# Kernel optimization log

Measured on AMD Instinct MI355X. Metric: run time of the kernel, lower is better.

Reference implementation:

```python
import jax, jax.numpy as jnp
import numpy as np

NEG_SLOPE = 0.2

def setup_inputs() -> dict:
    key = jax.random.key(0)
    ks = jax.random.split(key, 10)
    N, E, F, H, C, NC, G = 50000, 800000, 256, 8, 32, 10, 128
    x = jax.random.normal(ks[0], (N, F), jnp.float32)
    W1 = jax.random.normal(ks[1], (F, H * C), jnp.float32) * (1.0 / np.sqrt(F))
    a_src1 = jax.random.normal(ks[2], (H, C), jnp.float32) * 0.1
    a_dst1 = jax.random.normal(ks[3], (H, C), jnp.float32) * 0.1
    b1 = jnp.zeros((H * C,), jnp.float32)
    W2 = jax.random.normal(ks[4], (H * C, NC), jnp.float32) * (1.0 / np.sqrt(H * C))
    a_src2 = jax.random.normal(ks[5], (1, NC), jnp.float32) * 0.1
    a_dst2 = jax.random.normal(ks[6], (1, NC), jnp.float32) * 0.1
    b2 = jnp.zeros((NC,), jnp.float32)
    edge_index = jax.random.randint(ks[7], (2, E), 0, N, jnp.int64)
    batch = jnp.sort(jax.random.randint(ks[8], (N,), 0, G, jnp.int64))
    return {"x": x, "W1": W1, "a_src1": a_src1, "a_dst1": a_dst1, "b1": b1,
            "W2": W2, "a_src2": a_src2, "a_dst2": a_dst2, "b2": b2,
            "edge_index": edge_index, "batch": batch}


def gat_conv(x, W, a_src, a_dst, b, src, dst, concat):
    # x: [N,F] -> h: [N,H,C]
    N = x.shape[0]
    H, C = a_src.shape
    h = (x @ W).reshape(N, H, C)
    alpha_s = jnp.einsum('nhc,hc->nh', h, a_src)  # [N,H]
    alpha_d = jnp.einsum('nhc,hc->nh', h, a_dst)  # [N,H]
    e = jax.nn.leaky_relu(alpha_s[src] + alpha_d[dst], NEG_SLOPE)  # [E,H]
    # segment softmax over edges sharing the same destination node
    m = jax.ops.segment_max(e, dst, num_segments=N)
    ex = jnp.exp(e - m[dst])
    s = jax.ops.segment_sum(ex, dst, num_segments=N)
    alpha = ex / s[dst]
    msg = h[src] * alpha[:, :, None]  # [E,H,C]
    out = jax.ops.segment_sum(msg, dst, num_segments=N)  # [N,H,C]
    out = out.reshape(N, H * C) if concat else out.mean(axis=1)
    return out + b


def reference(x, W1, a_src1, a_dst1, b1, W2, a_src2, a_dst2, b2, edge_index, batch):
    N = x.shape[0]
    G = 128
    loop = jnp.arange(N, dtype=edge_index.dtype)
    src = jnp.concatenate([edge_index[0], loop])  # add self loops (PyG default)
    dst = jnp.concatenate([edge_index[1], loop])
    # dropout layers are identity at inference (training=False)
    h = jax.nn.elu(gat_conv(x, W1, a_src1, a_dst1, b1, src, dst, concat=True))
    out = gat_conv(h, W2, a_src2, a_dst2, b2, src, dst, concat=False)  # [N,NC]
    # global mean pool over graphs
    sums = jax.ops.segment_sum(out, batch, num_segments=G)
    cnt = jax.ops.segment_sum(jnp.ones((N,), out.dtype), batch, num_segments=G)
    return sums / jnp.maximum(cnt, 1.0)[:, None]
```

## Files before the change

kernel.cpp:

```cpp
#include <hip/hip_runtime.h>
#include <hip/hip_bf16.h>
#include <math.h>

#define N_NODES 50000
#define N_EDGES 800000
#define E_TOT   (N_EDGES + N_NODES)
#define NCLS 10
#define NGRP 128

#define NBKT 196
#define EPB  1024
#define NB1  ((E_TOT + EPB - 1) / EPB)

typedef __attribute__((ext_vector_type(8))) short bf16x8;
typedef __attribute__((ext_vector_type(4))) float f32x4;
typedef __attribute__((ext_vector_type(2))) float f32x2;

static __device__ __forceinline__ ushort f2bf(float f) {
  union { float f; unsigned u; } v; v.f = f;
  unsigned r = v.u + 0x7fffu + ((v.u >> 16) & 1u);
  return (ushort)(r >> 16);
}
static __device__ __forceinline__ unsigned char enc8(float v) {
  int p = __builtin_amdgcn_cvt_pk_fp8_f32(v, v, 0, false);
  return (unsigned char)(p & 0xFF);
}
static __device__ __forceinline__ void fma4p(float w, unsigned u, f32x2* a) {
  f32x2 w2; w2[0] = w; w2[1] = w;
  a[0] += w2 * __builtin_amdgcn_cvt_pk_f32_fp8(u, false);
  a[1] += w2 * __builtin_amdgcn_cvt_pk_f32_fp8(u, true);
}

#define CAST_BLOCKS 2048
#define NX4 (N_NODES * 64)
#define W1T_BASE CAST_BLOCKS
#define W2T_BASE (W1T_BASE + 64)
#define WA_BASE  (W2T_BASE + 1)
#define HIST_BASE (WA_BASE + 1)
#define PREP_BLOCKS (HIST_BASE + NB1)

__global__ __launch_bounds__(256) void prep_kernel(const float4* __restrict__ X4,
                                                   ushort4* __restrict__ Xb,
                                                   const float* __restrict__ W1,
                                                   ushort* __restrict__ W1t,
                                                   const float* __restrict__ W2,
                                                   ushort* __restrict__ W2tp,
                                                   const float* __restrict__ asrc1,
                                                   const float* __restrict__ adst1,
                                                   const int* __restrict__ ei,
                                                   int* __restrict__ histg) {
  int b = blockIdx.x;
  int tid = threadIdx.x;
  if (b < CAST_BLOCKS) {
    for (int i = b * 256 + tid; i < NX4; i += CAST_BLOCKS * 256) {
      float4 v = X4[i];
      ushort4 o;
      o.x = f2bf(v.x); o.y = f2bf(v.y); o.z = f2bf(v.z); o.w = f2bf(v.w);
      Xb[i] = o;
    }
  } else if (b < W2T_BASE) {
    __shared__ float t[32][33];
    int bb = b - W1T_BASE;
    int k0 = (bb >> 3) * 32, n0 = (bb & 7) * 32;
    int tx = tid & 31, ty = tid >> 5;
    for (int r = 0; r < 32; r += 8)
      t[ty + r][tx] = W1[(k0 + ty + r) * 256 + n0 + tx];
    __syncthreads();
    for (int r = 0; r < 32; r += 8)
      W1t[(n0 + ty + r) * 256 + k0 + tx] = f2bf(t[tx][ty + r]);
  } else if (b == W2T_BASE) {
    int k = tid;
#pragma unroll
    for (int c = 0; c < 16; ++c)
      W2tp[c * 256 + k] = (c < NCLS) ? f2bf(W2[k * NCLS + c]) : (ushort)0;
  } else if (b == WA_BASE) {
    int k = tid;
    const float* wrow = W1 + k * 256;
#pragma unroll
    for (int h = 0; h < 8; ++h) {
      float s = 0.f, d = 0.f;
#pragma unroll
      for (int c = 0; c < 32; ++c) {
        float w = wrow[h * 32 + c];
        s += w * asrc1[h * 32 + c];
        d += w * adst1[h * 32 + c];
      }
      W1t[(256 + h) * 256 + k] = f2bf(s);
      W1t[(264 + h) * 256 + k] = f2bf(d);
    }
  } else {
    __shared__ int h[NBKT];
    int bb = b - HIST_BASE;
    for (int j = tid; j < NBKT; j += 256) h[j] = 0;
    __syncthreads();
    int base = bb * EPB;
#pragma unroll
    for (int t = 0; t < 4; ++t) {
      int i = base + t * 256 + tid;
      if (i < E_TOT) {
        int d = (i < N_EDGES) ? ei[N_EDGES + i] : (i - N_EDGES);
        atomicAdd(&h[d >> 8], 1);
      }
    }
    __syncthreads();
    for (int j = tid; j < NBKT; j += 256) histg[j * NB1 + bb] = h[j];
  }
}

#define GEMM_BLOCKS ((N_NODES + 63) / 64)

__global__ __launch_bounds__(256) void gemm1_mfma(const ushort* __restrict__ Xb,
                                                  const ushort* __restrict__ W1t,
                                                  unsigned char* __restrict__ h1f8,
                                                  float* __restrict__ as1,
                                                  float* __restrict__ ad1) {
  __shared__ ushort As[32][64][8];
  int wid = threadIdx.x >> 6, lane = threadIdx.x & 63;
  int r = lane & 15, kg = lane >> 4;
  int m0 = blockIdx.x * 64;
  int n0 = wid * 64;
  bool extra = (wid == 3);

  {
    int mi = wid;
    int row = m0 + mi * 16 + r;
    if (row >= N_NODES) row = 0;
    const ushort* src = Xb + (size_t)row * 256 + kg * 8;
    bf16x8 v0 = *reinterpret_cast<const bf16x8*>(src);
    bf16x8 v1 = *reinterpret_cast<const bf16x8*>(src + 32);
    bf16x8 v2 = *reinterpret_cast<const bf16x8*>(src + 64);
    bf16x8 v3 = *reinterpret_cast<const bf16x8*>(src + 96);
    bf16x8 v4 = *reinterpret_cast<const bf16x8*>(src + 128);
    bf16x8 v5 = *reinterpret_cast<const bf16x8*>(src + 160);
    bf16x8 v6 = *reinterpret_cast<const bf16x8*>(src + 192);
    bf16x8 v7 = *reinterpret_cast<const bf16x8*>(src + 224);
    *reinterpret_cast<bf16x8*>(&As[mi * 8 + 0][lane][0]) = v0;
    *reinterpret_cast<bf16x8*>(&As[mi * 8 + 1][lane][0]) = v1;
    *reinterpret_cast<bf16x8*>(&As[mi * 8 + 2][lane][0]) = v2;
    *reinterpret_cast<bf16x8*>(&As[mi * 8 + 3][lane][0]) = v3;
    *reinterpret_cast<bf16x8*>(&As[mi * 8 + 4][lane][0]) = v4;
    *reinterpret_cast<bf16x8*>(&As[mi * 8 + 5][lane][0]) = v5;
    *reinterpret_cast<bf16x8*>(&As[mi * 8 + 6][lane][0]) = v6;
    *reinterpret_cast<bf16x8*>(&As[mi * 8 + 7][lane][0]) = v7;
  }
  __syncthreads();

  f32x4 acc[4][4];
  f32x4 accE[4];
#pragma unroll
  for (int mi = 0; mi < 4; ++mi) {
#pragma unroll
    for (int ni = 0; ni < 4; ++ni) acc[mi][ni] = 0;
    accE[mi] = 0;
  }

  const ushort* bptr[4];
#pragma unroll
  for (int ni = 0; ni < 4; ++ni)
    bptr[ni] = W1t + (size_t)(n0 + ni * 16 + r) * 256 + kg * 8;
  const ushort* bptrE = W1t + (size_t)(256 + r) * 256 + kg * 8;

#pragma unroll 2
  for (int ks = 0; ks < 8; ++ks) {
    int k0 = ks * 32;
    bf16x8 a[4], b[4], bE;
#pragma unroll
    for (int ni = 0; ni < 4; ++ni)
      b[ni] = *reinterpret_cast<const bf16x8*>(bptr[ni] + k0);
    if (extra) bE = *reinterpret_cast<const bf16x8*>(bptrE + k0);
#pragma unroll
    for (int mi = 0; mi < 4; ++mi)
      a[mi] = *reinterpret_cast<const bf16x8*>(&As[mi * 8 + ks][lane][0]);
#pragma unroll
    for (int mi = 0; mi < 4; ++mi) {
#pragma unroll
      for (int ni = 0; ni < 4; ++ni)
        acc[mi][ni] = __builtin_amdgcn_mfma_f32_16x16x32_bf16(a[mi], b[ni], acc[mi][ni], 0, 0, 0);
      if (extra)
        accE[mi] = __builtin_amdgcn_mfma_f32_16x16x32_bf16(a[mi], bE, accE[mi], 0, 0, 0);
    }
  }

#pragma unroll
  for (int mi = 0; mi < 4; ++mi) {
#pragma unroll
    for (int q = 0; q < 4; ++q) {
      int row = m0 + mi * 16 + kg * 4 + q;
      if (row < N_NODES) {
#pragma unroll
        for (int ni = 0; ni < 4; ++ni)
          h1f8[(size_t)row * 256 + n0 + ni * 16 + r] = enc8(acc[mi][ni][q]);
        if (extra) {
          float* dst = (r < 8) ? (as1 + row * 8 + r) : (ad1 + row * 8 + (r & 7));
          *dst = accE[mi][q];
        }
      }
    }
  }
}

__global__ __launch_bounds__(256) void k_scan(int* __restrict__ histg,
                                              int* __restrict__ tot) {
  __shared__ int sh[256];
  int b = blockIdx.x, tid = threadIdx.x;
  int carry = 0;
  for (int c = 0; c < (NB1 + 255) / 256; ++c) {
    int j = c * 256 + tid;
    int v = (j < NB1) ? histg[b * NB1 + j] : 0;
    sh[tid] = v;
    __syncthreads();
    for (int d = 1; d < 256; d <<= 1) {
      int t = (tid >= d) ? sh[tid - d] : 0;
      __syncthreads();
      sh[tid] += t;
      __syncthreads();
    }
    if (j < NB1) histg[b * NB1 + j] = carry + sh[tid] - v;
    carry += sh[255];
    __syncthreads();
  }
  if (tid == 0) tot[b] = carry;
}

__global__ __launch_bounds__(256) void k_base(const int* __restrict__ tot,
                                              int* __restrict__ baseg) {
  __shared__ int sh[256];
  int tid = threadIdx.x;
  int v = (tid < NBKT) ? tot[tid] : 0;
  sh[tid] = v;
  __syncthreads();
  for (int d = 1; d < 256; d <<= 1) {
    int t = (tid >= d) ? sh[tid - d] : 0;
    __syncthreads();
    sh[tid] += t;
    __syncthreads();
  }
  if (tid < NBKT) baseg[tid] = sh[tid] - v;
  if (tid == 255) baseg[NBKT] = sh[255];
}

__global__ __launch_bounds__(256) void k_place(const int* __restrict__ ei,
                                               const int* __restrict__ histg,
                                               const int* __restrict__ baseg,
                                               unsigned int* __restrict__ cs) {
  __shared__ int h[NBKT];
  __shared__ int basec[NBKT];
  int tid = threadIdx.x;
  for (int j = tid; j < NBKT; j += 256) {
    h[j] = 0;
    basec[j] = baseg[j] + histg[j * NB1 + blockIdx.x];
  }
  __syncthreads();
  int base = blockIdx.x * EPB;
#pragma unroll
  for (int t = 0; t < 4; ++t) {
    int i = base + t * 256 + tid;
    if (i < E_TOT) {
      int s = (i < N_EDGES) ? ei[i] : (i - N_EDGES);
      int d = (i < N_EDGES) ? ei[N_EDGES + i] : (i - N_EDGES);
      int bk = d >> 8;
      int r = atomicAdd(&h[bk], 1);
      cs[basec[bk] + r] = ((unsigned)d << 16) | (unsigned)s;
    }
  }
}

__global__ __launch_bounds__(256) void k_fine(const unsigned int* __restrict__ cs,
                                              const int* __restrict__ baseg,
                                              int* __restrict__ csr,
                                              int* __restrict__ off) {
  __shared__ int cnt[256];
  __shared__ int sh[256];
  __shared__ int scn[256];
  __shared__ int cur[256];
  int b = blockIdx.x, tid = threadIdx.x;
  int lo = baseg[b], hi = baseg[b + 1];
  cnt[tid] = 0;
  cur[tid] = 0;
  __syncthreads();
  for (int i = lo + tid; i < hi; i += 256) atomicAdd(&cnt[(cs[i] >> 16) & 255], 1);
  __syncthreads();
  int v = cnt[tid];
  sh[tid] = v;
  __syncthreads();
  for (int d = 1; d < 256; d <<= 1) {
    int t = (tid >= d) ? sh[tid - d] : 0;
    __syncthreads();
    sh[tid] += t;
    __syncthreads();
  }
  scn[tid] = sh[tid] - v;
  int idx = b * 256 + tid;
  if (idx <= N_NODES) off[idx] = lo + scn[tid];
  __syncthreads();
  for (int i = lo + tid; i < hi; i += 256) {
    unsigned e = cs[i];
    int dl = (e >> 16) & 255;
    int r = atomicAdd(&cur[dl], 1);
    csr[lo + scn[dl] + r] = (int)((e & 0xFFFFu) << 8);
  }
}

__global__ __launch_bounds__(256) void agg1_kernel(const unsigned char* __restrict__ h1f8,
                                                   const float* __restrict__ as1,
                                                   const float* __restrict__ ad1,
                                                   const int* __restrict__ off,
                                                   const int* __restrict__ csr,
                                                   const float* __restrict__ b1,
                                                   ushort* __restrict__ h2b) {
  int n = (blockIdx.x * 256 + threadIdx.x) >> 6;
  int lane = threadIdx.x & 63;
  int p0 = off[n], p1 = off[n + 1];

  int sl = lane >> 4;
  int cl = lane & 15;
  int cb = cl * 16;
  int h = cl >> 1;
  float ad = ad1[n * 8 + h];

  float ssum = 0.f;
  f32x2 acc2[8];
#pragma unroll
  for (int j = 0; j < 8; ++j) { acc2[j][0] = 0.f; acc2[j][1] = 0.f; }

  int p = p0 + sl;
  for (; p + 4 < p1; p += 8) {
    int vA = csr[p], vB = csr[p + 4];
    float eA = as1[(vA >> 5) + h] + ad;
    float eB = as1[(vB >> 5) + h] + ad;
    uint4 rA = *reinterpret_cast<const uint4*>(h1f8 + vA + cb);
    uint4 rB = *reinterpret_cast<const uint4*>(h1f8 + vB + cb);
    eA = eA > 0.f ? eA : 0.2f * eA;
    eB = eB > 0.f ? eB : 0.2f * eB;
    float wA = __expf(eA), wB = __expf(eB);
    ssum += wA + wB;
    fma4p(wA, rA.x, acc2 + 0); fma4p(wB, rB.x, acc2 + 0);
    fma4p(wA, rA.y, acc2 + 2); fma4p(wB, rB.y, acc2 + 2);
    fma4p(wA, rA.z, acc2 + 4); fma4p(wB, rB.z, acc2 + 4);
    fma4p(wA, rA.w, acc2 + 6); fma4p(wB, rB.w, acc2 + 6);
  }
  for (; p < p1; p += 4) {
    int vA = csr[p];
    float eA = as1[(vA >> 5) + h] + ad;
    uint4 rA = *reinterpret_cast<const uint4*>(h1f8 + vA + cb);
    eA = eA > 0.f ? eA : 0.2f * eA;
    float wA = __expf(eA);
    ssum += wA;
    fma4p(wA, rA.x, acc2 + 0);
    fma4p(wA, rA.y, acc2 + 2);
    fma4p(wA, rA.z, acc2 + 4);
    fma4p(wA, rA.w, acc2 + 6);
  }

  ssum += __shfl_xor(ssum, 16); ssum += __shfl_xor(ssum, 32);
#pragma unroll
  for (int j = 0; j < 8; ++j) {
    acc2[j][0] += __shfl_xor(acc2[j][0], 16);
    acc2[j][0] += __shfl_xor(acc2[j][0], 32);
    acc2[j][1] += __shfl_xor(acc2[j][1], 16);
    acc2[j][1] += __shfl_xor(acc2[j][1], 32);
  }

  if (sl == 0) {
    float inv = 1.f / ssum;
    float o[16];
    float4 b0 = *reinterpret_cast<const float4*>(b1 + cb);
    float4 b1v = *reinterpret_cast<const float4*>(b1 + cb + 4);
    float4 b2v = *reinterpret_cast<const float4*>(b1 + cb + 8);
    float4 b3v = *reinterpret_cast<const float4*>(b1 + cb + 12);
    float bb[16] = {b0.x, b0.y, b0.z, b0.w, b1v.x, b1v.y, b1v.z, b1v.w,
                    b2v.x, b2v.y, b2v.z, b2v.w, b3v.x, b3v.y, b3v.z, b3v.w};
#pragma unroll
    for (int c = 0; c < 16; ++c) {
      float v = acc2[c >> 1][c & 1] * inv + bb[c];
      o[c] = v > 0.f ? v : __expf(v) - 1.f;
    }
    int4 o0, o1;
    o0.x = (int)(((unsigned)f2bf(o[1]) << 16) | f2bf(o[0]));
    o0.y = (int)(((unsigned)f2bf(o[3]) << 16) | f2bf(o[2]));
    o0.z = (int)(((unsigned)f2bf(o[5]) << 16) | f2bf(o[4]));
    o0.w = (int)(((unsigned)f2bf(o[7]) << 16) | f2bf(o[6]));
    o1.x = (int)(((unsigned)f2bf(o[9]) << 16) | f2bf(o[8]));
    o1.y = (int)(((unsigned)f2bf(o[11]) << 16) | f2bf(o[10]));
    o1.z = (int)(((unsigned)f2bf(o[13]) << 16) | f2bf(o[12]));
    o1.w = (int)(((unsigned)f2bf(o[15]) << 16) | f2bf(o[14]));
    *reinterpret_cast<int4*>(h2b + (size_t)n * 256 + cb) = o0;
    *reinterpret_cast<int4*>(h2b + (size_t)n * 256 + cb + 8) = o1;
  }
}

__global__ __launch_bounds__(256) void proj2_mfma(const ushort* __restrict__ h2b,
                                                  const ushort* __restrict__ W2tp,
                                                  const float* __restrict__ asrc2,
                                                  const float* __restrict__ adst2,
                                                  float* __restrict__ pj2p,
                                                  float* __restrict__ as2,
                                                  float* __restrict__ ad2) {
  int wid = threadIdx.x >> 6, lane = threadIdx.x & 63;
  int r = lane & 15, kg = lane >> 4;
  int rb = blockIdx.x * 64 + wid * 16;
  int row_a = rb + r;
  if (row_a >= N_NODES) row_a = 0;
  const ushort* ap = h2b + (size_t)row_a * 256 + kg * 8;
  const ushort* bp = W2tp + (size_t)r * 256 + kg * 8;
  f32x4 acc = 0;
#pragma unroll
  for (int k0 = 0; k0 < 256; k0 += 32)
    acc = __builtin_amdgcn_mfma_f32_16x16x32_bf16(
        *reinterpret_cast<const bf16x8*>(ap + k0),
        *reinterpret_cast<const bf16x8*>(bp + k0), acc, 0, 0, 0);

  float av = (r < NCLS) ? asrc2[r] : 0.f;
  float dv = (r < NCLS) ? adst2[r] : 0.f;
#pragma unroll
  for (int q = 0; q < 4; ++q) {
    int row = rb + kg * 4 + q;
    float v = acc[q];
    if (row < N_NODES) pj2p[row * 16 + r] = v;
    float s = v * av, d = v * dv;
    s += __shfl_xor(s, 1); s += __shfl_xor(s, 2); s += __shfl_xor(s, 4); s += __shfl_xor(s, 8);
    d += __shfl_xor(d, 1); d += __shfl_xor(d, 2); d += __shfl_xor(d, 4); d += __shfl_xor(d, 8);
    if (r == 0 && row < N_NODES) { as2[row] = s; ad2[row] = d; }
  }
}

__global__ __launch_bounds__(256) void agg2_kernel(const float* __restrict__ pj2p,
                                                   const float* __restrict__ as2,
                                                   const float* __restrict__ ad2,
                                                   const int* __restrict__ off,
                                                   const int* __restrict__ csr,
                                                   const float* __restrict__ b2,
                                                   float* __restrict__ out2p) {
  int n = (blockIdx.x * 256 + threadIdx.x) >> 6;
  int lane = threadIdx.x & 63;
  int p0 = off[n], p1 = off[n + 1];
  float ad = ad2[n];
  int es = lane >> 4, c = lane & 15;
  float ssum = 0.f, acc = 0.f;
  int p = p0 + es;
  for (; p + 12 < p1; p += 16) {
    int v0 = csr[p], v1 = csr[p + 4], v2 = csr[p + 8], v3 = csr[p + 12];
    float e0 = as2[v0 >> 8] + ad, e1 = as2[v1 >> 8] + ad;
    float e2 = as2[v2 >> 8] + ad, e3 = as2[v3 >> 8] + ad;
    float q0 = pj2p[(v0 >> 4) + c], q1 = pj2p[(v1 >> 4) + c];
    float q2 = pj2p[(v2 >> 4) + c], q3 = pj2p[(v3 >> 4) + c];
    e0 = e0 > 0.f ? e0 : 0.2f * e0;
    e1 = e1 > 0.f ? e1 : 0.2f * e1;
    e2 = e2 > 0.f ? e2 : 0.2f * e2;
    e3 = e3 > 0.f ? e3 : 0.2f * e3;
    float w0 = __expf(e0), w1 = __expf(e1), w2 = __expf(e2), w3 = __expf(e3);
    ssum += (w0 + w1) + (w2 + w3);
    acc += (w0 * q0 + w1 * q1) + (w2 * q2 + w3 * q3);
  }
  for (; p < p1; p += 4) {
    int vA = csr[p];
    float eA = as2[vA >> 8] + ad;
    float qA = pj2p[(vA >> 4) + c];
    eA = eA > 0.f ? eA : 0.2f * eA;
    float wA = __expf(eA);
    ssum += wA;
    acc += wA * qA;
  }
  acc += __shfl_xor(acc, 16); acc += __shfl_xor(acc, 32);
  ssum += __shfl_xor(ssum, 16); ssum += __shfl_xor(ssum, 32);
  if (lane < 16) {
    float bc = (lane < NCLS) ? b2[lane] : 0.f;
    out2p[n * 16 + lane] = acc / ssum + bc;
  }
}

__global__ __launch_bounds__(256) void pool_kernel(const float* __restrict__ out2p,
                                                   const int* __restrict__ batch,
                                                   float* __restrict__ outp) {
  __shared__ float red[256];
  int g = blockIdx.x;
  int lo = 0, hi = N_NODES;
  while (lo < hi) { int mid = (lo + hi) >> 1; if (batch[mid] < g) lo = mid + 1; else hi = mid; }
  int start = lo;
  hi = N_NODES;
  while (lo < hi) { int mid = (lo + hi) >> 1; if (batch[mid] < g + 1) lo = mid + 1; else hi = mid; }
  int end = lo;
  int t = threadIdx.x;
  int c = t & 15, nsl = t >> 4;
  float loc = 0.f;
  for (int nn = start + nsl; nn < end; nn += 16) loc += out2p[nn * 16 + c];
  red[t] = loc;
  __syncthreads();
  for (int s = 128; s >= 16; s >>= 1) {
    if (t < s) red[t] += red[t + s];
    __syncthreads();
  }
  if (t < NCLS) {
    float denom = fmaxf((float)(end - start), 1.f);
    outp[g * NCLS + t] = red[t] / denom;
  }
}

extern "C" void kernel_launch(void* const* d_in, const int* in_sizes, int n_in,
                              void* d_out, int out_size, void* d_ws, size_t ws_size,
                              hipStream_t stream) {
  const float* x      = (const float*)d_in[0];
  const float* W1     = (const float*)d_in[1];
  const float* a_src1 = (const float*)d_in[2];
  const float* a_dst1 = (const float*)d_in[3];
  const float* b1     = (const float*)d_in[4];
  const float* W2     = (const float*)d_in[5];
  const float* a_src2 = (const float*)d_in[6];
  const float* a_dst2 = (const float*)d_in[7];
  const float* b2     = (const float*)d_in[8];
  const int*   ei     = (const int*)d_in[9];
  const int*   batch  = (const int*)d_in[10];

  char* ws = (char*)d_ws;
  size_t o = 0;
  auto alloc = [&](size_t bytes) {
    char* p = ws + o;
    o = (o + bytes + 255) & ~(size_t)255;
    return p;
  };
  ushort* xb   = (ushort*)alloc((size_t)N_NODES * 256 * 2);
  ushort* w1t  = (ushort*)alloc((size_t)272 * 256 * 2);
  ushort* w2tp = (ushort*)alloc((size_t)16 * 256 * 2);
  unsigned char* h1f8 = (unsigned char*)alloc((size_t)N_NODES * 256);
  ushort* h2b  = (ushort*)alloc((size_t)N_NODES * 256 * 2);
  float* as1   = (float*)alloc((size_t)N_NODES * 8 * 4);
  float* ad1   = (float*)alloc((size_t)N_NODES * 8 * 4);
  float* pj2p  = (float*)alloc((size_t)N_NODES * 16 * 4);
  float* as2   = (float*)alloc((size_t)N_NODES * 4);
  float* ad2   = (float*)alloc((size_t)N_NODES * 4);
  float* out2p = (float*)alloc((size_t)N_NODES * 16 * 4);
  int*   histg = (int*)alloc((size_t)NBKT * NB1 * 4);
  int*   tot   = (int*)alloc((size_t)NBKT * 4);
  int*   baseg = (int*)alloc((size_t)(NBKT + 1) * 4);
  unsigned int* cs = (unsigned int*)alloc((size_t)E_TOT * 4);
  int*   csr   = (int*)alloc((size_t)E_TOT * 4);
  int*   off   = (int*)alloc((size_t)(N_NODES + 1) * 4);

  prep_kernel<<<PREP_BLOCKS, 256, 0, stream>>>((const float4*)x, (ushort4*)xb,
                                               W1, w1t, W2, w2tp, a_src1, a_dst1,
                                               ei, histg);
  gemm1_mfma<<<GEMM_BLOCKS, 256, 0, stream>>>(xb, w1t, h1f8, as1, ad1);

  k_scan<<<NBKT, 256, 0, stream>>>(histg, tot);
  k_base<<<1, 256, 0, stream>>>(tot, baseg);
  k_place<<<NB1, 256, 0, stream>>>(ei, histg, baseg, cs);
  k_fine<<<NBKT, 256, 0, stream>>>(cs, baseg, csr, off);

  agg1_kernel<<<N_NODES / 4, 256, 0, stream>>>(h1f8, as1, ad1, off, csr, b1, h2b);
  proj2_mfma<<<GEMM_BLOCKS, 256, 0, stream>>>(h2b, w2tp, a_src2, a_dst2,
                                              pj2p, as2, ad2);
  agg2_kernel<<<N_NODES / 4, 256, 0, stream>>>(pj2p, as2, ad2, off, csr, b2, out2p);
  pool_kernel<<<NGRP, 256, 0, stream>>>(out2p, batch, (float*)d_out);
}
```

Before: 264.9 us.

## Fuse edge placement into GEMM launch and fold bucket-base scan into consumers

Removes the separate k_base and k_place launches. Each placement block and each k_fine block now recomputes the small 196-entry prefix scan of bucket totals, and the placement blocks are appended to the GEMM1 grid so the sort scatter can overlap with the MFMA work. The agg1 accumulation also switches from packed f32x2 FMAs to scalar FMAs on a 16-float array. The cost is redundant scans per block and mixed block types in one grid, which may affect occupancy or register use of the GEMM path.

```diff
diff --git a/kernel.cpp b/kernel.cpp
--- a/kernel.cpp
+++ b/kernel.cpp
@@ -25,10 +25,10 @@
   int p = __builtin_amdgcn_cvt_pk_fp8_f32(v, v, 0, false);
   return (unsigned char)(p & 0xFF);
 }
-static __device__ __forceinline__ void fma4p(float w, unsigned u, f32x2* a) {
-  f32x2 w2; w2[0] = w; w2[1] = w;
-  a[0] += w2 * __builtin_amdgcn_cvt_pk_f32_fp8(u, false);
-  a[1] += w2 * __builtin_amdgcn_cvt_pk_f32_fp8(u, true);
+static __device__ __forceinline__ void fma4(float w, unsigned u, float* a) {
+  f32x2 lo = __builtin_amdgcn_cvt_pk_f32_fp8(u, false);
+  f32x2 hi = __builtin_amdgcn_cvt_pk_f32_fp8(u, true);
+  a[0] += w * lo[0]; a[1] += w * lo[1]; a[2] += w * hi[0]; a[3] += w * hi[1];
 }
 
 #define CAST_BLOCKS 2048
@@ -107,15 +107,80 @@
   }
 }
 
+__global__ __launch_bounds__(256) void k_scan(int* __restrict__ histg,
+                                              int* __restrict__ tot) {
+  __shared__ int sh[256];
+  int b = blockIdx.x, tid = threadIdx.x;
+  int carry = 0;
+  for (int c = 0; c < (NB1 + 255) / 256; ++c) {
+    int j = c * 256 + tid;
+    int v = (j < NB1) ? histg[b * NB1 + j] : 0;
+    sh[tid] = v;
+    __syncthreads();
+    for (int d = 1; d < 256; d <<= 1) {
+      int t = (tid >= d) ? sh[tid - d] : 0;
+      __syncthreads();
+      sh[tid] += t;
+      __syncthreads();
+    }
+    if (j < NB1) histg[b * NB1 + j] = carry + sh[tid] - v;
+    carry += sh[255];
+    __syncthreads();
+  }
+  if (tid == 0) tot[b] = carry;
+}
+
 #define GEMM_BLOCKS ((N_NODES + 63) / 64)
-
-__global__ __launch_bounds__(256) void gemm1_mfma(const ushort* __restrict__ Xb,
+#define GP_BLOCKS (GEMM_BLOCKS + NB1)
+
+__global__ __launch_bounds__(256) void gemm_place(const ushort* __restrict__ Xb,
                                                   const ushort* __restrict__ W1t,
                                                   unsigned char* __restrict__ h1f8,
                                                   float* __restrict__ as1,
-                                                  float* __restrict__ ad1) {
+                                                  float* __restrict__ ad1,
+                                                  const int* __restrict__ ei,
+                                                  const int* __restrict__ histg,
+                                                  const int* __restrict__ tot,
+                                                  unsigned int* __restrict__ cs) {
   __shared__ ushort As[32][64][8];
-  int wid = threadIdx.x >> 6, lane = threadIdx.x & 63;
+  int tid = threadIdx.x;
+
+  if (blockIdx.x >= GEMM_BLOCKS) {
+    int bb = blockIdx.x - GEMM_BLOCKS;
+    int* L = (int*)As;
+    int* h     = L;
+    int* basec = L + 256;
+    int* sh    = L + 512;
+    int tv = (tid < NBKT) ? tot[tid] : 0;
+    sh[tid] = tv;
+    __syncthreads();
+    for (int d = 1; d < 256; d <<= 1) {
+      int t = (tid >= d) ? sh[tid - d] : 0;
+      __syncthreads();
+      sh[tid] += t;
+      __syncthreads();
+    }
+    if (tid < NBKT) {
+      basec[tid] = (sh[tid] - tv) + histg[tid * NB1 + bb];
+      h[tid] = 0;
+    }
+    __syncthreads();
+    int base = bb * EPB;
+#pragma unroll
+    for (int t = 0; t < 4; ++t) {
+      int i = base + t * 256 + tid;
+      if (i < E_TOT) {
+        int s = (i < N_EDGES) ? ei[i] : (i - N_EDGES);
+        int d = (i < N_EDGES) ? ei[N_EDGES + i] : (i - N_EDGES);
+        int bk = d >> 8;
+        int r = atomicAdd(&h[bk], 1);
+        cs[basec[bk] + r] = ((unsigned)d << 16) | (unsigned)s;
+      }
+    }
+    return;
+  }
+
+  int wid = tid >> 6, lane = tid & 63;
   int r = lane & 15, kg = lane >> 4;
   int m0 = blockIdx.x * 64;
   int n0 = wid * 64;
@@ -199,74 +264,8 @@
   }
 }
 
-__global__ __launch_bounds__(256) void k_scan(int* __restrict__ histg,
-                                              int* __restrict__ tot) {
-  __shared__ int sh[256];
-  int b = blockIdx.x, tid = threadIdx.x;
-  int carry = 0;
-  for (int c = 0; c < (NB1 + 255) / 256; ++c) {
-    int j = c * 256 + tid;
-    int v = (j < NB1) ? histg[b * NB1 + j] : 0;
-    sh[tid] = v;
-    __syncthreads();
-    for (int d = 1; d < 256; d <<= 1) {
-      int t = (tid >= d) ? sh[tid - d] : 0;
-      __syncthreads();
-      sh[tid] += t;
-      __syncthreads();
-    }
-    if (j < NB1) histg[b * NB1 + j] = carry + sh[tid] - v;
-    carry += sh[255];
-    __syncthreads();
-  }
-  if (tid == 0) tot[b] = carry;
-}
-
-__global__ __launch_bounds__(256) void k_base(const int* __restrict__ tot,
-                                              int* __restrict__ baseg) {
-  __shared__ int sh[256];
-  int tid = threadIdx.x;
-  int v = (tid < NBKT) ? tot[tid] : 0;
-  sh[tid] = v;
-  __syncthreads();
-  for (int d = 1; d < 256; d <<= 1) {
-    int t = (tid >= d) ? sh[tid - d] : 0;
-    __syncthreads();
-    sh[tid] += t;
-    __syncthreads();
-  }
-  if (tid < NBKT) baseg[tid] = sh[tid] - v;
-  if (tid == 255) baseg[NBKT] = sh[255];
-}
-
-__global__ __launch_bounds__(256) void k_place(const int* __restrict__ ei,
-                                               const int* __restrict__ histg,
-                                               const int* __restrict__ baseg,
-                                               unsigned int* __restrict__ cs) {
-  __shared__ int h[NBKT];
-  __shared__ int basec[NBKT];
-  int tid = threadIdx.x;
-  for (int j = tid; j < NBKT; j += 256) {
-    h[j] = 0;
-    basec[j] = baseg[j] + histg[j * NB1 + blockIdx.x];
-  }
-  __syncthreads();
-  int base = blockIdx.x * EPB;
-#pragma unroll
-  for (int t = 0; t < 4; ++t) {
-    int i = base + t * 256 + tid;
-    if (i < E_TOT) {
-      int s = (i < N_EDGES) ? ei[i] : (i - N_EDGES);
-      int d = (i < N_EDGES) ? ei[N_EDGES + i] : (i - N_EDGES);
-      int bk = d >> 8;
-      int r = atomicAdd(&h[bk], 1);
-      cs[basec[bk] + r] = ((unsigned)d << 16) | (unsigned)s;
-    }
-  }
-}
-
 __global__ __launch_bounds__(256) void k_fine(const unsigned int* __restrict__ cs,
-                                              const int* __restrict__ baseg,
+                                              const int* __restrict__ tot,
                                               int* __restrict__ csr,
                                               int* __restrict__ off) {
   __shared__ int cnt[256];
@@ -274,7 +273,20 @@
   __shared__ int scn[256];
   __shared__ int cur[256];
   int b = blockIdx.x, tid = threadIdx.x;
-  int lo = baseg[b], hi = baseg[b + 1];
+
+  int tv = (tid < NBKT) ? tot[tid] : 0;
+  sh[tid] = tv;
+  __syncthreads();
+  for (int d = 1; d < 256; d <<= 1) {
+    int t = (tid >= d) ? sh[tid - d] : 0;
+    __syncthreads();
+    sh[tid] += t;
+    __syncthreads();
+  }
+  int hi = sh[b];
+  int lo = hi - tot[b];
+  __syncthreads();
+
   cnt[tid] = 0;
   cur[tid] = 0;
   __syncthreads();
@@ -319,9 +331,7 @@
   float ad = ad1[n * 8 + h];
 
   float ssum = 0.f;
-  f32x2 acc2[8];
-#pragma unroll
-  for (int j = 0; j < 8; ++j) { acc2[j][0] = 0.f; acc2[j][1] = 0.f; }
+  float acc[16] = {};
 
   int p = p0 + sl;
   for (; p + 4 < p1; p += 8) {
@@ -334,10 +344,10 @@
     eB = eB > 0.f ? eB : 0.2f * eB;
     float wA = __expf(eA), wB = __expf(eB);
     ssum += wA + wB;
-    fma4p(wA, rA.x, acc2 + 0); fma4p(wB, rB.x, acc2 + 0);
-    fma4p(wA, rA.y, acc2 + 2); fma4p(wB, rB.y, acc2 + 2);
-    fma4p(wA, rA.z, acc2 + 4); fma4p(wB, rB.z, acc2 + 4);
-    fma4p(wA, rA.w, acc2 + 6); fma4p(wB, rB.w, acc2 + 6);
+    fma4(wA, rA.x, acc);      fma4(wB, rB.x, acc);
+    fma4(wA, rA.y, acc + 4);  fma4(wB, rB.y, acc + 4);
+    fma4(wA, rA.z, acc + 8);  fma4(wB, rB.z, acc + 8);
+    fma4(wA, rA.w, acc + 12); fma4(wB, rB.w, acc + 12);
   }
   for (; p < p1; p += 4) {
     int vA = csr[p];
@@ -346,19 +356,17 @@
     eA = eA > 0.f ? eA : 0.2f * eA;
     float wA = __expf(eA);
     ssum += wA;
-    fma4p(wA, rA.x, acc2 + 0);
-    fma4p(wA, rA.y, acc2 + 2);
-    fma4p(wA, rA.z, acc2 + 4);
-    fma4p(wA, rA.w, acc2 + 6);
+    fma4(wA, rA.x, acc);
+    fma4(wA, rA.y, acc + 4);
+    fma4(wA, rA.z, acc + 8);
+    fma4(wA, rA.w, acc + 12);
   }
 
   ssum += __shfl_xor(ssum, 16); ssum += __shfl_xor(ssum, 32);
 #pragma unroll
-  for (int j = 0; j < 8; ++j) {
-    acc2[j][0] += __shfl_xor(acc2[j][0], 16);
-    acc2[j][0] += __shfl_xor(acc2[j][0], 32);
-    acc2[j][1] += __shfl_xor(acc2[j][1], 16);
-    acc2[j][1] += __shfl_xor(acc2[j][1], 32);
+  for (int c = 0; c < 16; ++c) {
+    acc[c] += __shfl_xor(acc[c], 16);
+    acc[c] += __shfl_xor(acc[c], 32);
   }
 
   if (sl == 0) {
@@ -372,7 +380,7 @@
                     b2v.x, b2v.y, b2v.z, b2v.w, b3v.x, b3v.y, b3v.z, b3v.w};
 #pragma unroll
     for (int c = 0; c < 16; ++c) {
-      float v = acc2[c >> 1][c & 1] * inv + bb[c];
+      float v = acc[c] * inv + bb[c];
       o[c] = v > 0.f ? v : __expf(v) - 1.f;
     }
     int4 o0, o1;
@@ -531,7 +539,6 @@
   float* out2p = (float*)alloc((size_t)N_NODES * 16 * 4);
   int*   histg = (int*)alloc((size_t)NBKT * NB1 * 4);
   int*   tot   = (int*)alloc((size_t)NBKT * 4);
-  int*   baseg = (int*)alloc((size_t)(NBKT + 1) * 4);
   unsigned int* cs = (unsigned int*)alloc((size_t)E_TOT * 4);
   int*   csr   = (int*)alloc((size_t)E_TOT * 4);
   int*   off   = (int*)alloc((size_t)(N_NODES + 1) * 4);
@@ -539,12 +546,10 @@
   prep_kernel<<<PREP_BLOCKS, 256, 0, stream>>>((const float4*)x, (ushort4*)xb,
                                                W1, w1t, W2, w2tp, a_src1, a_dst1,
                                                ei, histg);
-  gemm1_mfma<<<GEMM_BLOCKS, 256, 0, stream>>>(xb, w1t, h1f8, as1, ad1);
-
   k_scan<<<NBKT, 256, 0, stream>>>(histg, tot);
-  k_base<<<1, 256, 0, stream>>>(tot, baseg);
-  k_place<<<NB1, 256, 0, stream>>>(ei, histg, baseg, cs);
-  k_fine<<<NBKT, 256, 0, stream>>>(cs, baseg, csr, off);
+  gemm_place<<<GP_BLOCKS, 256, 0, stream>>>(xb, w1t, h1f8, as1, ad1,
+                                            ei, histg, tot, cs);
+  k_fine<<<NBKT, 256, 0, stream>>>(cs, tot, csr, off);
 
   agg1_kernel<<<N_NODES / 4, 256, 0, stream>>>(h1f8, as1, ad1, off, csr, b1, h2b);
   proj2_mfma<<<GEMM_BLOCKS, 256, 0, stream>>>(h2b, w2tp, a_src2, a_dst2,
```

New measurement: 261.2 us. Within noise of the previous version (-1.4%).
